# Performance work log

Hardware: AMD Instinct MI355X
Metric: run time of the kernel (lower is better)

The kernel has to match this reference:

```python
import jax, jax.numpy as jnp
import numpy as np

B, L, E = 512, 50, 512
VOCAB = 32000
EPS = 1e-5


def setup_inputs() -> dict:
    key = jax.random.key(0)
    ks = jax.random.split(key, 16)
    inp = {
        'src_tokens': jax.random.randint(ks[0], (B, L), 0, VOCAB, dtype=jnp.int32),
        'trg_tokens': jax.random.randint(ks[1], (B, L), 0, VOCAB, dtype=jnp.int32),
        'pad_idx': 1,
        'emb_src': jax.random.normal(ks[2], (VOCAB, E), jnp.float32) * 0.02,
        'emb_trg': jax.random.normal(ks[3], (VOCAB, E), jnp.float32) * 0.02,
        'W1': jax.random.normal(ks[4], (20, E), jnp.float32) / np.sqrt(E),  # Conv1d(1,20,k=E) kernel squeezed
        'b1': jax.random.normal(ks[5], (20,), jnp.float32) * 0.01,
        'g1': jnp.ones((20,), jnp.float32),
        'beta1': jnp.zeros((20,), jnp.float32),
        'W2': jax.random.normal(ks[6], (40, 20, 3, 3), jnp.float32) / np.sqrt(20 * 9),
        'b2': jax.random.normal(ks[7], (40,), jnp.float32) * 0.01,
        'g2': jnp.ones((40,), jnp.float32),
        'beta2': jnp.zeros((40,), jnp.float32),
        'Wfc1': jax.random.normal(ks[8], (20, 40 * 11 * 11), jnp.float32) / np.sqrt(40 * 11 * 11),
        'bfc1': jnp.zeros((20,), jnp.float32),
        'Wfc2': jax.random.normal(ks[9], (1, 20), jnp.float32) / np.sqrt(20),
        'bfc2': jnp.zeros((1,), jnp.float32),
    }
    return inp


def _maxpool2(x):  # [B,C,H,W] -> 2x2/2 valid max pool
    return jax.lax.reduce_window(x, -jnp.inf, jax.lax.max, (1, 1, 2, 2), (1, 1, 2, 2), 'VALID')


def reference(src_tokens, trg_tokens, pad_idx, emb_src, emb_trg, W1, b1, g1, beta1,
              W2, b2, g2, beta2, Wfc1, bfc1, Wfc2, bfc2):
    src_e = emb_src[src_tokens]  # [B,L,E]
    trg_e = emb_trg[trg_tokens]  # [B,L,E]

    def conv1_bn_relu(x):
        # per-sample Conv1d(1,20,k=E): collapses E -> scalar per position/channel
        f = jnp.einsum('ble,ce->blc', x, W1) + b1  # [B,L,20]
        # per-sample BatchNorm1d in training mode: stats over the L positions of each sample
        mu = jnp.mean(f, axis=1, keepdims=True)
        var = jnp.var(f, axis=1, keepdims=True)  # biased, as torch uses for normalization
        f = (f - mu) * jax.lax.rsqrt(var + EPS) * g1 + beta1
        return jax.nn.relu(f)

    s = conv1_bn_relu(src_e)  # [B,L,20]
    t = conv1_bn_relu(trg_e)  # [B,L,20]

    # broadcast outer-sum: out[b,i,j,c] = s[b,j,c] + t[b,i,c]
    out = s[:, None, :, :] + t[:, :, None, :]          # [B,L,L,20]
    out = jnp.transpose(out, (0, 3, 1, 2))             # [B,20,L,L]
    out = _maxpool2(out)                                # [B,20,25,25]

    out = jax.lax.conv_general_dilated(out, W2, (1, 1), 'VALID') + b2[None, :, None, None]  # [B,40,23,23]
    # BatchNorm2d training mode: stats over (batch, H, W)
    mu = jnp.mean(out, axis=(0, 2, 3), keepdims=True)
    var = jnp.var(out, axis=(0, 2, 3), keepdims=True)
    out = (out - mu) * jax.lax.rsqrt(var + EPS) * g2[None, :, None, None] + beta2[None, :, None, None]
    out = jax.nn.relu(out)
    out = _maxpool2(out)                                # [B,40,11,11]

    out = out.reshape(out.shape[0], -1)                 # [B,4840]
    out = out @ Wfc1.T + bfc1
    out = out @ Wfc2.T + bfc2
    return jax.nn.sigmoid(out)                          # [B,1]
```

## Files before the change

kernel.cpp:

```cpp
#include <hip/hip_runtime.h>
#include <hip/hip_bf16.h>

#define EPS 1e-5f

__device__ __forceinline__ float bf2f(unsigned short u) {
  union { unsigned int i; float f; } x; x.i = ((unsigned int)u) << 16; return x.f;
}
__device__ __forceinline__ float loadp(const void* p, int i, bool f32) {
  return f32 ? ((const float*)p)[i] : bf2f(((const unsigned short*)p)[i]);
}
__device__ __forceinline__ bool detect_f32(const void* g1) {
  return ((const unsigned int*)g1)[0] == 0x3F800000u;
}

__global__ __launch_bounds__(256) void k0_prep(
    const void* __restrict__ W1, const void* __restrict__ W2,
    const void* __restrict__ Wfc1,
    const void* __restrict__ g1, const void* __restrict__ beta1,
    const void* __restrict__ g2, const void* __restrict__ beta2,
    const void* __restrict__ bfc1, const void* __restrict__ Wfc2,
    const void* __restrict__ bfc2,
    float* __restrict__ W1T, float* __restrict__ WT, float* __restrict__ WS,
    float* __restrict__ Wfc1T, float* __restrict__ prm)
{
  const bool f32 = detect_f32(g1);
  int g = blockIdx.x * 256 + threadIdx.x;
  const int NT = 64 * 256;
  for (int i = g; i < 512 * 20; i += NT) {
    int e = i / 20, c = i - e * 20;
    W1T[i] = loadp(W1, c * 512 + e, f32);
  }
  for (int i = g; i < 40 * 3 * 20; i += NT) {
    int o = i / 60, r = i - o * 60;
    int k = r / 20, c = r - k * 20;
    float st = 0.f, ss = 0.f;
    for (int q = 0; q < 3; ++q) {
      st += loadp(W2, ((o * 20 + c) * 3 + k) * 3 + q, f32);
      ss += loadp(W2, ((o * 20 + c) * 3 + q) * 3 + k, f32);
    }
    WT[(o * 3 + k) * 20 + c] = st;
    WS[(o * 3 + k) * 20 + c] = ss;
  }
  for (int i = g; i < 4840 * 20; i += NT) {
    int kk = i / 4840, idx = i - kk * 4840;
    Wfc1T[idx * 20 + kk] = loadp(Wfc1, i, f32);
  }
  if (g < 20)        prm[g] = loadp(g1,    g,       f32);
  else if (g < 40)   prm[g] = loadp(beta1, g - 20,  f32);
  else if (g < 80)   prm[g] = loadp(g2,    g - 40,  f32);
  else if (g < 120)  prm[g] = loadp(beta2, g - 80,  f32);
  else if (g < 140)  prm[g] = loadp(bfc1,  g - 120, f32);
  else if (g < 160)  prm[g] = loadp(Wfc2,  g - 140, f32);
  else if (g == 160) prm[g] = loadp(bfc2,  0,       f32);
}

__global__ __launch_bounds__(256, 6) void k12_fused(
    const int* __restrict__ src_tok, const int* __restrict__ trg_tok,
    const void* __restrict__ emb_src, const void* __restrict__ emb_trg,
    const void* __restrict__ g1flag,
    const float* __restrict__ W1T,
    const float* __restrict__ WT, const float* __restrict__ WS,
    const float* __restrict__ prm,
    float* __restrict__ C1, float* __restrict__ R, float* __restrict__ S2)
{
  __shared__ float lds[4200];

  const bool f32 = detect_f32(g1flag);
  int bb = blockIdx.x;
  int side = bb >> 9, b = bb & 511;
  int t = threadIdx.x;
  int lane = t & 63;
  int ch = __builtin_amdgcn_readfirstlane(t >> 6);

  float acc[20];
#pragma unroll
  for (int c = 0; c < 20; ++c) acc[c] = 0.f;
  if (lane < 50) {
    int tok = side ? trg_tok[b * 50 + lane] : src_tok[b * 50 + lane];
    const void* emb = side ? emb_trg : emb_src;
    if (f32) {
      const float4* rowp = (const float4*)((const float*)emb + (size_t)tok * 512 + ch * 128);
      for (int grp = 0; grp < 4; ++grp) {
        float4 u[8];
#pragma unroll
        for (int q = 0; q < 8; ++q) u[q] = rowp[grp * 8 + q];
        __builtin_amdgcn_sched_barrier(0);
#pragma unroll
        for (int q = 0; q < 8; ++q) {
          float v[4] = { u[q].x, u[q].y, u[q].z, u[q].w };
          const float* w = W1T + (ch * 128 + grp * 32 + q * 4) * 20;
#pragma unroll
          for (int j = 0; j < 4; ++j)
#pragma unroll
            for (int c = 0; c < 20; ++c) acc[c] = fmaf(v[j], w[j * 20 + c], acc[c]);
        }
      }
    } else {
      const uint4* rowp = (const uint4*)((const unsigned short*)emb + (size_t)tok * 512 + ch * 128);
      for (int half = 0; half < 2; ++half) {
        uint4 u[8];
#pragma unroll
        for (int q = 0; q < 8; ++q) u[q] = rowp[half * 8 + q];
        __builtin_amdgcn_sched_barrier(0);
#pragma unroll
        for (int q = 0; q < 8; ++q) {
          const unsigned int* qu = (const unsigned int*)&u[q];
          float v[8];
#pragma unroll
          for (int j = 0; j < 4; ++j) {
            union { unsigned int i; float f; } lo, hi;
            lo.i = qu[j] << 16; hi.i = qu[j] & 0xffff0000u;
            v[2 * j] = lo.f; v[2 * j + 1] = hi.f;
          }
          const float* w = W1T + (ch * 128 + half * 64 + q * 8) * 20;
#pragma unroll
          for (int j = 0; j < 8; ++j)
#pragma unroll
            for (int c = 0; c < 20; ++c) acc[c] = fmaf(v[j], w[j * 20 + c], acc[c]);
        }
      }
    }
    float* pp = &lds[(ch * 50 + lane) * 21];
#pragma unroll
    for (int c = 0; c < 20; ++c) pp[c] = acc[c];
  }
  __syncthreads();
  for (int i = t; i < 1000; i += 256) {
    int l = i / 20, c = i - l * 20;
    float s = lds[l * 21 + c] + lds[(50 + l) * 21 + c]
            + lds[(100 + l) * 21 + c] + lds[(150 + l) * 21 + c];
    lds[l * 21 + c] = s;
  }
  __syncthreads();
  {
    const float* wsrc = side ? WT : WS;
    for (int i = t; i < 2400; i += 256) lds[1050 + i] = wsrc[i];
  }
  if (t < 20) {
    float s = 0.f, s2 = 0.f;
#pragma unroll
    for (int l = 0; l < 50; ++l) { float v = lds[l * 21 + t]; s += v; s2 += v * v; }
    float mu = s * (1.0f / 50.0f);
    float var = s2 * (1.0f / 50.0f) - mu * mu;
    float k = prm[t] * rsqrtf(var + EPS);
    lds[3975 + t] = k;
    lds[3995 + t] = prm[20 + t] - k * mu;
  }
  __syncthreads();
  for (int i = t; i < 500; i += 256) {
    int p = i / 20, c = i - p * 20;
    float k = lds[3975 + c], s0 = lds[3995 + c];
    float v0 = fmaxf(k * lds[(2 * p) * 21 + c] + s0, 0.f);
    float v1 = fmaxf(k * lds[(2 * p + 1) * 21 + c] + s0, 0.f);
    lds[3450 + p * 21 + c] = fmaxf(v0, v1);
  }
  __syncthreads();
  for (int i = t; i < 920; i += 256) {
    int o = i / 23, y = i - o * 23;
    float a = 0.f;
#pragma unroll
    for (int ky = 0; ky < 3; ++ky) {
      const float* wr = &lds[1050 + (o * 3 + ky) * 20];
      const float* pr = &lds[3450 + (y + ky) * 21];
#pragma unroll
      for (int c = 0; c < 20; ++c) a = fmaf(wr[c], pr[c], a);
    }
    C1[(size_t)bb * 920 + i] = a;
    lds[i] = a;
  }
  __syncthreads();
  if (t < 40) {
    float s = 0.f, s2 = 0.f;
#pragma unroll
    for (int y = 0; y < 23; ++y) { float v = lds[t * 23 + y]; s += v; s2 += v * v; }
    R[bb * 40 + t] = s;
    S2[bb * 40 + t] = s2;
  }
}

__global__ __launch_bounds__(256) void k3_bn2(
    const float* __restrict__ R, const float* __restrict__ S2,
    const float* __restrict__ prm,
    float* __restrict__ bn2)
{
  int o = blockIdx.x, t = threadIdx.x;
  float s1a = 0, s2a = 0, s1b = 0, s2b = 0, sab = 0;
  for (int b = t; b < 512; b += 256) {
    float ra = R[(512 + b) * 40 + o], rb = R[b * 40 + o];
    s1a += ra; s1b += rb; sab += ra * rb;
    s2a += S2[(512 + b) * 40 + o];
    s2b += S2[b * 40 + o];
  }
  __shared__ float Rd[5][256];
  Rd[0][t] = s1a; Rd[1][t] = s2a; Rd[2][t] = s1b; Rd[3][t] = s2b; Rd[4][t] = sab;
  __syncthreads();
  for (int s = 128; s > 0; s >>= 1) {
    if (t < s) {
#pragma unroll
      for (int q = 0; q < 5; ++q) Rd[q][t] += Rd[q][t + s];
    }
    __syncthreads();
  }
  if (t == 0) {
    const float invN = 1.0f / (512.0f * 23.0f);
    float muA = Rd[0][0] * invN, muB = Rd[2][0] * invN;
    float ea2 = Rd[1][0] * invN - muA * muA;
    float eb2 = Rd[3][0] * invN - muB * muB;
    float cross = 2.0f * (Rd[4][0] * (1.0f / (529.0f * 512.0f)) - muA * muB);
    float var = ea2 + eb2 + cross;
    float k = prm[40 + o] * rsqrtf(var + EPS);
    bn2[o] = k;
    bn2[40 + o] = prm[80 + o] - k * (muA + muB);
  }
}

__global__ __launch_bounds__(512) void k4_fc(
    const float* __restrict__ C1,
    const float* __restrict__ bn2,
    const float* __restrict__ Wfc1T,
    const float* __restrict__ prm,
    const void* __restrict__ g1flag,
    void* __restrict__ outv)
{
  const bool f32 = detect_f32(g1flag);
  int b = blockIdx.x, t = threadIdx.x;
  int lane = t & 63, wv = t >> 6;
  __shared__ float mA[440], mB[440];
  __shared__ float k2s[40], c2s[40];
  __shared__ float wred[8][20];
  __shared__ float o1[20];
  if (t < 40) k2s[t] = bn2[t];
  else if (t < 80) c2s[t - 40] = bn2[t];
  __syncthreads();
  for (int i = t; i < 440; i += 512) {
    int o = i / 11, y = i - o * 11;
    const float* pa = C1 + (size_t)(512 + b) * 920 + o * 23;
    const float* pb = C1 + (size_t)b * 920 + o * 23;
    float a0 = pa[2 * y], a1 = pa[2 * y + 1];
    float b0 = pb[2 * y], b1 = pb[2 * y + 1];
    if (k2s[o] >= 0.f) { mA[i] = fmaxf(a0, a1); mB[i] = fmaxf(b0, b1); }
    else               { mA[i] = fminf(a0, a1); mB[i] = fminf(b0, b1); }
  }
  __syncthreads();
  float acc[20];
#pragma unroll
  for (int c = 0; c < 20; ++c) acc[c] = 0.f;
  for (int idx = t; idx < 4840; idx += 512) {
    int o = idx / 121, r = idx - o * 121;
    int y = r / 11, x = r - y * 11;
    float p = fmaxf(k2s[o] * (mA[o * 11 + y] + mB[o * 11 + x]) + c2s[o], 0.f);
    const float* w = Wfc1T + idx * 20;
#pragma unroll
    for (int c = 0; c < 20; ++c) acc[c] = fmaf(p, w[c], acc[c]);
  }
#pragma unroll
  for (int c = 0; c < 20; ++c) {
    float v = acc[c];
    v += __shfl_xor(v, 32); v += __shfl_xor(v, 16); v += __shfl_xor(v, 8);
    v += __shfl_xor(v, 4);  v += __shfl_xor(v, 2);  v += __shfl_xor(v, 1);
    acc[c] = v;
  }
  if (lane == 0) {
#pragma unroll
    for (int c = 0; c < 20; ++c) wred[wv][c] = acc[c];
  }
  __syncthreads();
  if (t < 20) {
    float s = 0.f;
#pragma unroll
    for (int q = 0; q < 8; ++q) s += wred[q][t];
    o1[t] = s + prm[120 + t];
  }
  __syncthreads();
  if (t == 0) {
    float z = prm[160];
#pragma unroll
    for (int c = 0; c < 20; ++c) z = fmaf(prm[140 + c], o1[c], z);
    float sg = 1.0f / (1.0f + expf(-z));
    if (f32) ((float*)outv)[b] = sg;
    else     ((__hip_bfloat16*)outv)[b] = __float2bfloat16(sg);
  }
}

extern "C" void kernel_launch(void* const* d_in, const int* in_sizes, int n_in,
                              void* d_out, int out_size, void* d_ws, size_t ws_size,
                              hipStream_t stream) {
  const int* src_tok = (const int*)d_in[0];
  const int* trg_tok = (const int*)d_in[1];
  const void* emb_src = d_in[3];
  const void* emb_trg = d_in[4];
  const void* W1    = d_in[5];
  const void* g1    = d_in[7];
  const void* beta1 = d_in[8];
  const void* W2    = d_in[9];
  const void* g2    = d_in[11];
  const void* beta2 = d_in[12];
  const void* Wfc1  = d_in[13];
  const void* bfc1  = d_in[14];
  const void* Wfc2  = d_in[15];
  const void* bfc2  = d_in[16];

  char* ws = (char*)d_ws;
  float* W1T   = (float*)(ws + 0);
  float* WT    = (float*)(ws + 40960);
  float* WS    = (float*)(ws + 50560);
  float* Wfc1T = (float*)(ws + 60160);
  float* prm   = (float*)(ws + 447360);
  float* bn2   = (float*)(ws + 448384);
  float* R     = (float*)(ws + 448896);
  float* S2    = (float*)(ws + 612736);
  float* C1    = (float*)(ws + 776576);

  k0_prep<<<64, 256, 0, stream>>>(W1, W2, Wfc1, g1, beta1, g2, beta2, bfc1, Wfc2,
                                  bfc2, W1T, WT, WS, Wfc1T, prm);
  k12_fused<<<1024, 256, 0, stream>>>(src_tok, trg_tok, emb_src, emb_trg, g1,
                                      W1T, WT, WS, prm, C1, R, S2);
  k3_bn2<<<40, 256, 0, stream>>>(R, S2, prm, bn2);
  k4_fc<<<512, 512, 0, stream>>>(C1, bn2, Wfc1T, prm, g1, d_out);
}
```

Before: 206.7 us.

## Stream embedding rows into LDS via async global_load_lds with double buffering

Replaces per-lane register loads of each token's embedding row with asynchronous global_load_lds DMA into a double-buffered, XOR-swizzled LDS staging area. Each wave then computes its slice of the conv1 reduction out of LDS while the next chunk is in flight. Conv2 weights are prefetched into registers up front so their latency overlaps the gather, and the LDS layout is re-planned around the larger footprint. Shared memory grows to about 51 KB and occupancy hint drops to 3 blocks per CU, trading occupancy for explicit pipelining with hand-placed waitcnt and barriers.

Result: slower. 228.0 us (+10.3%).

```diff
diff --git a/kernel.cpp b/kernel.cpp
--- a/kernel.cpp
+++ b/kernel.cpp
@@ -2,6 +2,11 @@
 #include <hip/hip_bf16.h>
 
 #define EPS 1e-5f
+
+#define AS1 __attribute__((address_space(1)))
+#define AS3 __attribute__((address_space(3)))
+#define CFENCE() asm volatile("" ::: "memory")
+#define SBAR()   asm volatile("s_barrier" ::: "memory")
 
 __device__ __forceinline__ float bf2f(unsigned short u) {
   union { unsigned int i; float f; } x; x.i = ((unsigned int)u) << 16; return x.f;
@@ -54,7 +59,7 @@
   else if (g == 160) prm[g] = loadp(bfc2,  0,       f32);
 }
 
-__global__ __launch_bounds__(256, 6) void k12_fused(
+__global__ __launch_bounds__(256, 3) void k12_fused(
     const int* __restrict__ src_tok, const int* __restrict__ trg_tok,
     const void* __restrict__ emb_src, const void* __restrict__ emb_trg,
     const void* __restrict__ g1flag,
@@ -63,7 +68,7 @@
     const float* __restrict__ prm,
     float* __restrict__ C1, float* __restrict__ R, float* __restrict__ S2)
 {
-  __shared__ float lds[4200];
+  __shared__ __align__(16) float lds[12864];
 
   const bool f32 = detect_f32(g1flag);
   int bb = blockIdx.x;
@@ -72,96 +77,160 @@
   int lane = t & 63;
   int ch = __builtin_amdgcn_readfirstlane(t >> 6);
 
+  if (t < 50) {
+    const int* tp = side ? trg_tok : src_tok;
+    ((int*)lds)[12800 + t] = tp[b * 50 + t];
+  }
+  __syncthreads();
+
+  const int* tokl = (const int*)lds + 12800;
+  const char* embb = (const char*)(side ? emb_trg : emb_src);
+  const size_t rowbytes = f32 ? 2048 : 1024;
+
+  float wlreg[10];
+  {
+    const float* wsrc = side ? WT : WS;
+#pragma unroll
+    for (int q = 0; q < 10; ++q) {
+      int i = t + q * 256;
+      wlreg[q] = (i < 2400) ? wsrc[i] : 0.f;
+    }
+  }
+  CFENCE();
+
+  auto issue_chunk = [&](int j, int buf) {
+    for (int r = ch; r < 25; r += 4) {
+      int row = 2 * r + (lane >> 5);
+      int tok = tokl[row];
+      const char* g = embb + (size_t)tok * rowbytes + (size_t)(j * 512)
+                    + (((lane & 31) ^ (row & 7)) << 4);
+      __builtin_amdgcn_global_load_lds((const AS1 unsigned int*)g,
+          (AS3 unsigned int*)(lds + buf * 6400 + r * 256), 16, 0, 0);
+    }
+    CFENCE();
+  };
+  auto wait_chunk = [&]() {
+    if (ch == 0) asm volatile("s_waitcnt vmcnt(7)" ::: "memory");
+    else         asm volatile("s_waitcnt vmcnt(6)" ::: "memory");
+    __builtin_amdgcn_sched_barrier(0);
+  };
+
   float acc[20];
 #pragma unroll
   for (int c = 0; c < 20; ++c) acc[c] = 0.f;
-  if (lane < 50) {
-    int tok = side ? trg_tok[b * 50 + lane] : src_tok[b * 50 + lane];
-    const void* emb = side ? emb_trg : emb_src;
-    if (f32) {
-      const float4* rowp = (const float4*)((const float*)emb + (size_t)tok * 512 + ch * 128);
-      for (int grp = 0; grp < 4; ++grp) {
-        float4 u[8];
-#pragma unroll
-        for (int q = 0; q < 8; ++q) u[q] = rowp[grp * 8 + q];
-        __builtin_amdgcn_sched_barrier(0);
-#pragma unroll
-        for (int q = 0; q < 8; ++q) {
-          float v[4] = { u[q].x, u[q].y, u[q].z, u[q].w };
-          const float* w = W1T + (ch * 128 + grp * 32 + q * 4) * 20;
-#pragma unroll
-          for (int j = 0; j < 4; ++j)
-#pragma unroll
-            for (int c = 0; c < 20; ++c) acc[c] = fmaf(v[j], w[j * 20 + c], acc[c]);
+  const int l = lane;
+  const int lx = l & 7;
+
+  auto compute_f32 = [&](int j) {
+    if (l < 50) {
+      const float* bp = lds + (j & 1) * 6400 + l * 128;
+      const float* wq = W1T + (j * 128 + ch * 32) * 20;
+#pragma unroll
+      for (int k = 0; k < 8; ++k) {
+        const float4 v = *(const float4*)(bp + (ch * 8 + (k ^ lx)) * 4);
+        const float* w = wq + k * 80;
+        float vv[4] = { v.x, v.y, v.z, v.w };
+#pragma unroll
+        for (int jj = 0; jj < 4; ++jj)
+#pragma unroll
+          for (int c = 0; c < 20; ++c) acc[c] = fmaf(vv[jj], w[jj * 20 + c], acc[c]);
+      }
+    }
+  };
+  auto compute_bf16 = [&](int j) {
+    if (l < 50) {
+      const char* bp = (const char*)(lds + (j & 1) * 6400) + l * 512;
+      const float* wq = W1T + (j * 256 + ch * 64) * 20;
+#pragma unroll
+      for (int k = 0; k < 8; ++k) {
+        const uint4 u = *(const uint4*)(bp + (ch * 8 + (k ^ lx)) * 16);
+        const unsigned int* qu = (const unsigned int*)&u;
+        const float* w = wq + k * 160;
+#pragma unroll
+        for (int d = 0; d < 4; ++d) {
+          union { unsigned int i; float f; } lo, hi;
+          lo.i = qu[d] << 16; hi.i = qu[d] & 0xffff0000u;
+#pragma unroll
+          for (int c = 0; c < 20; ++c) acc[c] = fmaf(lo.f, w[(2 * d) * 20 + c], acc[c]);
+#pragma unroll
+          for (int c = 0; c < 20; ++c) acc[c] = fmaf(hi.f, w[(2 * d + 1) * 20 + c], acc[c]);
         }
       }
-    } else {
-      const uint4* rowp = (const uint4*)((const unsigned short*)emb + (size_t)tok * 512 + ch * 128);
-      for (int half = 0; half < 2; ++half) {
-        uint4 u[8];
-#pragma unroll
-        for (int q = 0; q < 8; ++q) u[q] = rowp[half * 8 + q];
-        __builtin_amdgcn_sched_barrier(0);
-#pragma unroll
-        for (int q = 0; q < 8; ++q) {
-          const unsigned int* qu = (const unsigned int*)&u[q];
-          float v[8];
-#pragma unroll
-          for (int j = 0; j < 4; ++j) {
-            union { unsigned int i; float f; } lo, hi;
-            lo.i = qu[j] << 16; hi.i = qu[j] & 0xffff0000u;
-            v[2 * j] = lo.f; v[2 * j + 1] = hi.f;
-          }
-          const float* w = W1T + (ch * 128 + half * 64 + q * 8) * 20;
-#pragma unroll
-          for (int j = 0; j < 8; ++j)
-#pragma unroll
-            for (int c = 0; c < 20; ++c) acc[c] = fmaf(v[j], w[j * 20 + c], acc[c]);
-        }
-      }
-    }
-    float* pp = &lds[(ch * 50 + lane) * 21];
+    }
+  };
+
+  if (f32) {
+    issue_chunk(0, 0); issue_chunk(1, 1);
+    wait_chunk(); SBAR();
+    compute_f32(0); SBAR();
+    issue_chunk(2, 0);
+    wait_chunk(); SBAR();
+    compute_f32(1); SBAR();
+    issue_chunk(3, 1);
+    wait_chunk(); SBAR();
+    compute_f32(2); SBAR();
+    asm volatile("s_waitcnt vmcnt(0)" ::: "memory");
+    __builtin_amdgcn_sched_barrier(0);
+    SBAR();
+    compute_f32(3);
+  } else {
+    issue_chunk(0, 0); issue_chunk(1, 1);
+    wait_chunk(); SBAR();
+    compute_bf16(0); SBAR();
+    asm volatile("s_waitcnt vmcnt(0)" ::: "memory");
+    __builtin_amdgcn_sched_barrier(0);
+    SBAR();
+    compute_bf16(1);
+  }
+
+  if (l < 50) {
+    float* pp = &lds[(ch * 50 + l) * 21];
 #pragma unroll
     for (int c = 0; c < 20; ++c) pp[c] = acc[c];
   }
   __syncthreads();
+
   for (int i = t; i < 1000; i += 256) {
-    int l = i / 20, c = i - l * 20;
-    float s = lds[l * 21 + c] + lds[(50 + l) * 21 + c]
-            + lds[(100 + l) * 21 + c] + lds[(150 + l) * 21 + c];
-    lds[l * 21 + c] = s;
-  }
-  __syncthreads();
-  {
-    const float* wsrc = side ? WT : WS;
-    for (int i = t; i < 2400; i += 256) lds[1050 + i] = wsrc[i];
-  }
+    int ll = i / 20, c = i - ll * 20;
+    float s = lds[ll * 21 + c] + lds[(50 + ll) * 21 + c]
+            + lds[(100 + ll) * 21 + c] + lds[(150 + ll) * 21 + c];
+    lds[4200 + ll * 21 + c] = s;
+  }
+#pragma unroll
+  for (int q = 0; q < 10; ++q) {
+    int i = t + q * 256;
+    if (i < 2400) lds[6400 + i] = wlreg[q];
+  }
+  __syncthreads();
+
   if (t < 20) {
     float s = 0.f, s2 = 0.f;
 #pragma unroll
-    for (int l = 0; l < 50; ++l) { float v = lds[l * 21 + t]; s += v; s2 += v * v; }
+    for (int ll = 0; ll < 50; ++ll) { float v = lds[4200 + ll * 21 + t]; s += v; s2 += v * v; }
     float mu = s * (1.0f / 50.0f);
     float var = s2 * (1.0f / 50.0f) - mu * mu;
     float k = prm[t] * rsqrtf(var + EPS);
-    lds[3975 + t] = k;
-    lds[3995 + t] = prm[20 + t] - k * mu;
-  }
-  __syncthreads();
+    lds[9330 + t] = k;
+    lds[9350 + t] = prm[20 + t] - k * mu;
+  }
+  __syncthreads();
+
   for (int i = t; i < 500; i += 256) {
     int p = i / 20, c = i - p * 20;
-    float k = lds[3975 + c], s0 = lds[3995 + c];
-    float v0 = fmaxf(k * lds[(2 * p) * 21 + c] + s0, 0.f);
-    float v1 = fmaxf(k * lds[(2 * p + 1) * 21 + c] + s0, 0.f);
-    lds[3450 + p * 21 + c] = fmaxf(v0, v1);
-  }
-  __syncthreads();
+    float k = lds[9330 + c], s0 = lds[9350 + c];
+    float v0 = fmaxf(k * lds[4200 + (2 * p) * 21 + c] + s0, 0.f);
+    float v1 = fmaxf(k * lds[4200 + (2 * p + 1) * 21 + c] + s0, 0.f);
+    lds[8800 + p * 21 + c] = fmaxf(v0, v1);
+  }
+  __syncthreads();
+
   for (int i = t; i < 920; i += 256) {
     int o = i / 23, y = i - o * 23;
     float a = 0.f;
 #pragma unroll
     for (int ky = 0; ky < 3; ++ky) {
-      const float* wr = &lds[1050 + (o * 3 + ky) * 20];
-      const float* pr = &lds[3450 + (y + ky) * 21];
+      const float* wr = &lds[6400 + (o * 3 + ky) * 20];
+      const float* pr = &lds[8800 + (y + ky) * 21];
 #pragma unroll
       for (int c = 0; c < 20; ++c) a = fmaf(wr[c], pr[c], a);
     }
@@ -169,6 +238,7 @@
     lds[i] = a;
   }
   __syncthreads();
+
   if (t < 40) {
     float s = 0.f, s2 = 0.f;
 #pragma unroll
```
